# Performance work log

Hardware: AMD Instinct MI355X
Metric: run time of the kernel (lower is better)

Reference implementation:

```python
import jax, jax.numpy as jnp
import numpy as np

DIM = 1024
NUM_HEADS = 16
HEAD_DIM = DIM // NUM_HEADS
SCALE = HEAD_DIM ** -0.5


def setup_inputs() -> dict:
    key = jax.random.key(0)
    ks = jax.random.split(key, 5)
    B, N, C = 2, 2048, DIM
    x = jax.random.normal(ks[0], (B, N, C), dtype=jnp.float32)
    s = 1.0 / np.sqrt(C)
    W_qkv = jax.random.normal(ks[1], (C, 3 * C), dtype=jnp.float32) * s
    b_qkv = jax.random.normal(ks[2], (3 * C,), dtype=jnp.float32) * 0.01
    W_proj = jax.random.normal(ks[3], (C, C), dtype=jnp.float32) * s
    b_proj = jax.random.normal(ks[4], (C,), dtype=jnp.float32) * 0.01
    return {"x": x, "W_qkv": W_qkv, "b_qkv": b_qkv, "W_proj": W_proj, "b_proj": b_proj}


def reference(x, W_qkv, b_qkv, W_proj, b_proj):
    B, N, C = x.shape
    qkv = x @ W_qkv + b_qkv                      # [B, N, 3C]
    qkv = qkv.reshape(B, N, 3, NUM_HEADS, HEAD_DIM)
    qkv = jnp.transpose(qkv, (2, 0, 3, 1, 4))    # [3, B, H, N, hd]
    # Faithful to source quirk: q = k = v = qkv[2]
    v = qkv[2]
    q = v
    k = v
    attn = jnp.einsum('bhnd,bhmd->bhnm', q, k) * SCALE
    attn = jax.nn.softmax(attn, axis=-1)
    out = jnp.einsum('bhnm,bhmd->bhnd', attn, v)  # [B, H, N, hd]
    out = jnp.transpose(out, (0, 2, 1, 3)).reshape(B, N, C)
    return out @ W_proj + b_proj
```

## Files before the change

### kernel.cpp

```cpp
#include <hip/hip_runtime.h>

typedef __bf16    bf16x4 __attribute__((ext_vector_type(4)));
typedef __bf16    bf16x8 __attribute__((ext_vector_type(8)));
typedef _Float16  f16x2  __attribute__((ext_vector_type(2)));
typedef _Float16  f16x4  __attribute__((ext_vector_type(4)));
typedef _Float16  f16x8  __attribute__((ext_vector_type(8)));
typedef float     f32x4  __attribute__((ext_vector_type(4)));

#define MFMA16x16x32 __builtin_amdgcn_mfma_f32_16x16x32_bf16
#define MFMA16x16x16F __builtin_amdgcn_mfma_f32_16x16x16f16

__device__ __forceinline__ void gload_lds16(const void* g, void* l) {
  __builtin_amdgcn_global_load_lds((const __attribute__((address_space(1))) void*)g,
                                   (__attribute__((address_space(3))) void*)l, 16, 0, 0);
}

__device__ __forceinline__ f16x2 pkrtz(float a, float b) {
  return __builtin_bit_cast(f16x2, __builtin_amdgcn_cvt_pkrtz(a, b));
}

__global__ __launch_bounds__(256) void prep_transpose(const float* __restrict__ Wqkv,
                                                      const float* __restrict__ Wproj,
                                                      __bf16* __restrict__ WvT,
                                                      __bf16* __restrict__ WpT) {
  __shared__ float tile[64][65];
  const float* src; __bf16* dst; int ld, c0;
  if (blockIdx.z == 0) { src = Wqkv; dst = WvT; ld = 3072; c0 = 2048; }
  else                 { src = Wproj; dst = WpT; ld = 1024; c0 = 0; }
  const int k0 = blockIdx.x * 64, n0 = blockIdx.y * 64;
  const int t = threadIdx.x;
#pragma unroll
  for (int i = 0; i < 4; i++) {
    int idx = t + i * 256; int r = idx >> 4, g = idx & 15;
    float4 v = *(const float4*)&src[(size_t)(k0 + r) * ld + c0 + n0 + g * 4];
    tile[r][g * 4 + 0] = v.x; tile[r][g * 4 + 1] = v.y;
    tile[r][g * 4 + 2] = v.z; tile[r][g * 4 + 3] = v.w;
  }
  __syncthreads();
#pragma unroll
  for (int i = 0; i < 4; i++) {
    int idx = t + i * 256; int n = idx >> 4, g = idx & 15;
    bf16x4 o;
    o.x = (__bf16)tile[g * 4 + 0][n]; o.y = (__bf16)tile[g * 4 + 1][n];
    o.z = (__bf16)tile[g * 4 + 2][n]; o.w = (__bf16)tile[g * 4 + 3][n];
    *(bf16x4*)&dst[(size_t)(n0 + n) * 1024 + k0 + g * 4] = o;
  }
}

__global__ __launch_bounds__(256, 4) void gemm_v(const float* __restrict__ x,
                                                 const __bf16* __restrict__ WvT,
                                                 const float* __restrict__ bias,
                                                 __bf16* __restrict__ V,
                                                 _Float16* __restrict__ Vt) {
  constexpr int K = 1024;
  __shared__ char lds[2 * 12288];
  const int t = threadIdx.x, w = t >> 6, l = t & 63, lr = l & 15, quad = l >> 4;
  const int m0 = blockIdx.x * 64, n0 = blockIdx.y * 64;

  const int rmA = t >> 3;
  const int kgAs = (t & 7) ^ (rmA & 7);
  const float* pA0 = x + (size_t)(m0 + rmA) * K + kgAs * 4;
  const float* pA1 = pA0 + (size_t)32 * K;
  const int rnB = t >> 2, kgB = t & 3;
  const __bf16* pB = WvT + (size_t)(n0 + rnB) * K + kgB * 8;

  f32x4 acc[4] = {};
  {
    char* buf = (char*)lds;
    gload_lds16(pA0, buf + t * 16);
    gload_lds16(pA1, buf + (t + 256) * 16);
    gload_lds16(pB, buf + 8192 + t * 16);
  }
  const int rr = w * 16 + lr;
  const int ga0 = rr * 8 + ((2 * quad) ^ (rr & 7));
  const int ga1 = rr * 8 + ((2 * quad + 1) ^ (rr & 7));
  for (int it = 0; it < 32; ++it) {
    __syncthreads();
    if (it + 1 < 32) {
      pA0 += 32; pA1 += 32; pB += 32;
      char* buf = (char*)lds + ((it + 1) & 1) * 12288;
      gload_lds16(pA0, buf + t * 16);
      gload_lds16(pA1, buf + (t + 256) * 16);
      gload_lds16(pB, buf + 8192 + t * 16);
    }
    const char* Abuf = (char*)lds + (it & 1) * 12288;
    const char* Bbuf = Abuf + 8192;
    f32x4 a0 = *(const f32x4*)(Abuf + ga0 * 16);
    f32x4 a1 = *(const f32x4*)(Abuf + ga1 * 16);
    bf16x8 af;
    af[0] = (__bf16)a0[0]; af[1] = (__bf16)a0[1]; af[2] = (__bf16)a0[2]; af[3] = (__bf16)a0[3];
    af[4] = (__bf16)a1[0]; af[5] = (__bf16)a1[1]; af[6] = (__bf16)a1[2]; af[7] = (__bf16)a1[3];
#pragma unroll
    for (int nc = 0; nc < 4; nc++) {
      bf16x8 bv = *(const bf16x8*)(Bbuf + (nc * 16 + lr) * 64 + quad * 16);
      acc[nc] = MFMA16x16x32(af, bv, acc[nc], 0, 0, 0);
    }
  }
  const int b_ = blockIdx.x >> 5, by = blockIdx.y;
  const int ntok0 = (m0 & 2047) + w * 16 + quad * 4;
#pragma unroll
  for (int nc = 0; nc < 4; nc++) {
    int gcol = n0 + nc * 16 + lr;
    float bb = bias[gcol];
    float v0 = acc[nc][0] + bb, v1 = acc[nc][1] + bb;
    float v2 = acc[nc][2] + bb, v3 = acc[nc][3] + bb;
#pragma unroll
    for (int r = 0; r < 4; r++) {
      int grow = m0 + w * 16 + quad * 4 + r;
      float vv = (r == 0) ? v0 : (r == 1) ? v1 : (r == 2) ? v2 : v3;
      V[(size_t)grow * 1024 + gcol] = (__bf16)vv;
    }
    f16x2 lo = pkrtz(v0, v1), hi = pkrtz(v2, v3);
    f16x4 pv; pv[0] = lo[0]; pv[1] = lo[1]; pv[2] = hi[0]; pv[3] = hi[1];
    *(f16x4*)&Vt[((size_t)(b_ * 16 + by) * 64 + nc * 16 + lr) * 2048 + ntok0] = pv;
  }
}

__global__ __launch_bounds__(256, 4) void gemm_proj(const __bf16* __restrict__ A,
                                                    const __bf16* __restrict__ Bt,
                                                    const float* __restrict__ bias,
                                                    float* __restrict__ outp) {
  constexpr int K = 1024, Nn = 1024;
  __shared__ __bf16 lds[2 * 4096];
  const int t = threadIdx.x, w = t >> 6, l = t & 63, lr = l & 15, quad = l >> 4;
  const int m0 = blockIdx.x * 64, n0 = blockIdx.y * 64;
  const int rm = t >> 2, kg = t & 3;

  const __bf16* pA = A  + (size_t)(m0 + rm) * K + kg * 8;
  const __bf16* pB = Bt + (size_t)(n0 + rm) * K + kg * 8;

  f32x4 acc[4] = {};
  gload_lds16(pA, (char*)lds + t * 16);
  gload_lds16(pB, (char*)lds + 4096 + t * 16);
  for (int it = 0; it < 32; ++it) {
    __syncthreads();
    if (it + 1 < 32) {
      pA += 32; pB += 32;
      char* buf = (char*)lds + ((it + 1) & 1) * 8192;
      gload_lds16(pA, buf + t * 16);
      gload_lds16(pB, buf + 4096 + t * 16);
    }
    const __bf16* Al = lds + (it & 1) * 4096;
    const __bf16* Bl = Al + 2048;
    bf16x8 af = *(const bf16x8*)&Al[(w * 16 + lr) * 32 + quad * 8];
#pragma unroll
    for (int nc = 0; nc < 4; nc++) {
      bf16x8 bv = *(const bf16x8*)&Bl[(nc * 16 + lr) * 32 + quad * 8];
      acc[nc] = MFMA16x16x32(af, bv, acc[nc], 0, 0, 0);
    }
  }
#pragma unroll
  for (int nc = 0; nc < 4; nc++)
#pragma unroll
    for (int r = 0; r < 4; r++) {
      int grow = m0 + w * 16 + quad * 4 + r;
      int gcol = n0 + nc * 16 + lr;
      outp[(size_t)grow * Nn + gcol] = acc[nc][r] + bias[gcol];
    }
}

__global__ __launch_bounds__(512, 4) void attn_kernel(const __bf16* __restrict__ V,
                                                      const _Float16* __restrict__ Vt,
                                                      __bf16* __restrict__ O) {
  __shared__ char lds[65536];
  const int t = threadIdx.x, w = t >> 6, l = t & 63, lr = l & 15, quad = l >> 4;
  const int bh = blockIdx.x, b = bh >> 4, h = bh & 15;
  const int qb = blockIdx.y * 128 + (w & 3) * 16;
  const int part = w >> 2;

  const __bf16* Vbh = V + (size_t)b * 2048 * 1024 + h * 64;
  const _Float16* Vtbh = Vt + (size_t)bh * 64 * 2048;

  bf16x8 qf[2][2];
#pragma unroll
  for (int sub = 0; sub < 2; sub++)
#pragma unroll
    for (int ks = 0; ks < 2; ks++)
      qf[sub][ks] = *(const bf16x8*)(Vbh + (size_t)(qb + sub * 64 + lr) * 1024 + ks * 32 + quad * 8);

  const int kva = t >> 3, ua = (t & 7) ^ (kva & 7);
  const __bf16* pK0 = Vbh + (size_t)kva * 1024 + ua * 8;
  const __bf16* pK1 = pK0 + (size_t)64 * 1024;
  const int kb_ = t >> 7, d_ = (t >> 1) & 63, qh = (t & 1) ^ ((d_ >> 2) & 1);
  const _Float16* pV0 = Vtbh + (size_t)d_ * 2048 + kb_ * 16 + qh * 8;
  const _Float16* pV1 = pV0 + 64;

  const int koff0 = lr * 128 + ((quad ^ (lr & 7)) * 16);
  const int koff1 = lr * 128 + (((4 + quad) ^ (lr & 7)) * 16);
  const int xq = (quad >> 1) ^ ((lr >> 2) & 1);
  const int voff = lr * 32 + xq * 16 + (quad & 1) * 8;

  f32x4 o[2][4] = {};
  f32x4 l5[2] = {};
  f16x4 ones; ones[0] = ones[1] = ones[2] = ones[3] = (_Float16)1.0f;
  const float Cc = 0.18033688011112042f;
  const float C8 = 11.541560327111707f;

  {
    char* base = lds;
    gload_lds16(pK0, base + t * 16);
    gload_lds16(pV0, base + 8192 + t * 16);
    gload_lds16(pK1, base + 16384 + t * 16);
    gload_lds16(pV1, base + 24576 + t * 16);
  }
  for (int it = 0; it < 16; ++it) {
    __syncthreads();
    if (it + 1 < 16) {
      pK0 += 131072; pK1 += 131072; pV0 += 128; pV1 += 128;
      char* base = lds + ((it + 1) & 1) * 32768;
      gload_lds16(pK0, base + t * 16);
      gload_lds16(pV0, base + 8192 + t * 16);
      gload_lds16(pK1, base + 16384 + t * 16);
      gload_lds16(pV1, base + 24576 + t * 16);
    }
    const char* Kb = lds + (it & 1) * 32768 + part * 16384;
    const char* Vb = Kb + 8192;

    f32x4 s[2][4] = {};
#pragma unroll
    for (int ks = 0; ks < 2; ks++) {
      const int ko = ks ? koff1 : koff0;
#pragma unroll
      for (int rb = 0; rb < 4; rb++) {
        bf16x8 kf = *(const bf16x8*)(Kb + ko + rb * 2048);
        s[0][rb] = MFMA16x16x32(kf, qf[0][ks], s[0][rb], 0, 0, 0);
        s[1][rb] = MFMA16x16x32(kf, qf[1][ks], s[1][rb], 0, 0, 0);
      }
    }

    f16x4 pf[2][4];
#pragma unroll
    for (int sub = 0; sub < 2; sub++)
#pragma unroll
      for (int rb = 0; rb < 4; rb++) {
        float p0 = __builtin_amdgcn_exp2f(s[sub][rb][0] * Cc - C8);
        float p1 = __builtin_amdgcn_exp2f(s[sub][rb][1] * Cc - C8);
        float p2 = __builtin_amdgcn_exp2f(s[sub][rb][2] * Cc - C8);
        float p3 = __builtin_amdgcn_exp2f(s[sub][rb][3] * Cc - C8);
        f16x2 lo = pkrtz(p0, p1);
        f16x2 hi = pkrtz(p2, p3);
        pf[sub][rb][0] = lo[0]; pf[sub][rb][1] = lo[1];
        pf[sub][rb][2] = hi[0]; pf[sub][rb][3] = hi[1];
      }

#pragma unroll
    for (int kb = 0; kb < 4; kb++) {
#pragma unroll
      for (int db = 0; db < 4; db++) {
        f16x4 vf = *(const f16x4*)(Vb + voff + db * 512 + kb * 2048);
        o[0][db] = MFMA16x16x16F(pf[0][kb], vf, o[0][db], 0, 0, 0);
        o[1][db] = MFMA16x16x16F(pf[1][kb], vf, o[1][db], 0, 0, 0);
      }
      l5[0] = MFMA16x16x16F(pf[0][kb], ones, l5[0], 0, 0, 0);
      l5[1] = MFMA16x16x16F(pf[1][kb], ones, l5[1], 0, 0, 0);
    }
  }

  __syncthreads();
  float* xch = (float*)lds;
  if (w >= 4) {
    float* dsto = xch + (w - 4) * 2048;
#pragma unroll
    for (int sub = 0; sub < 2; sub++)
#pragma unroll
      for (int db = 0; db < 4; db++)
        *(f32x4*)&dsto[(sub * 4 + db) * 256 + l * 4] = o[sub][db];
    float* dstl = xch + 8192 + (w - 4) * 512;
    *(f32x4*)&dstl[l * 4] = l5[0];
    *(f32x4*)&dstl[256 + l * 4] = l5[1];
  }
  __syncthreads();
  if (w < 4) {
    const float* srco = xch + w * 2048;
    const float* srcl = xch + 8192 + w * 512;
#pragma unroll
    for (int sub = 0; sub < 2; sub++) {
#pragma unroll
      for (int db = 0; db < 4; db++)
        o[sub][db] += *(const f32x4*)&srco[(sub * 4 + db) * 256 + l * 4];
      l5[sub] += *(const f32x4*)&srcl[sub * 256 + l * 4];
    }
#pragma unroll
    for (int sub = 0; sub < 2; sub++)
#pragma unroll
      for (int r = 0; r < 4; r++) {
        float lv = 1.0f / l5[sub][r];
        int token = b * 2048 + qb + sub * 64 + quad * 4 + r;
#pragma unroll
        for (int db = 0; db < 4; db++)
          O[(size_t)token * 1024 + h * 64 + db * 16 + lr] = (__bf16)(o[sub][db][r] * lv);
      }
  }
}

extern "C" void kernel_launch(void* const* d_in, const int* in_sizes, int n_in,
                              void* d_out, int out_size, void* d_ws, size_t ws_size,
                              hipStream_t stream) {
  (void)in_sizes; (void)n_in; (void)out_size; (void)ws_size;
  const float* x     = (const float*)d_in[0];
  const float* Wqkv  = (const float*)d_in[1];
  const float* bqkv  = (const float*)d_in[2];
  const float* Wproj = (const float*)d_in[3];
  const float* bproj = (const float*)d_in[4];

  char* ws = (char*)d_ws;
  __bf16*    V   = (__bf16*)(ws);
  _Float16*  Vt  = (_Float16*)(ws + (size_t)8  * 1048576);
  __bf16*    Ob  = (__bf16*)(ws + (size_t)16 * 1048576);
  __bf16*    WvT = (__bf16*)(ws + (size_t)24 * 1048576);
  __bf16*    WpT = (__bf16*)(ws + (size_t)26 * 1048576);

  prep_transpose<<<dim3(16, 16, 2), 256, 0, stream>>>(Wqkv, Wproj, WvT, WpT);
  gemm_v<<<dim3(64, 16), 256, 0, stream>>>(x, WvT, bqkv + 2048, V, Vt);
  attn_kernel<<<dim3(32, 16), 512, 0, stream>>>(V, Vt, Ob);
  gemm_proj<<<dim3(64, 16), 256, 0, stream>>>(Ob, WpT, bproj, (float*)d_out);
}
```

Measured before the change: 165.1 us.

## Fuse all four stages into one persistent cooperative kernel with grid syncs

Replaces the four separate launches (weight transpose, V GEMM, attention, projection GEMM) with a single cooperative kernel of 256 blocks of 512 threads. Each phase is separated by grid.sync, and each block loops over two work tiles per phase. The GEMM tiles are retiled to 128x64. The aim is to remove launch gaps and kernel tail effects. The cost is grid-wide barriers, only 256 resident blocks, and a fallback to the old launches if the cooperative launch fails.

```diff
diff --git a/kernel.cpp b/kernel.cpp
--- a/kernel.cpp
+++ b/kernel.cpp
@@ -1,10 +1,11 @@
 #include <hip/hip_runtime.h>
+#include <hip/hip_cooperative_groups.h>
+namespace cg = cooperative_groups;
 
 typedef __bf16    bf16x4 __attribute__((ext_vector_type(4)));
 typedef __bf16    bf16x8 __attribute__((ext_vector_type(8)));
 typedef _Float16  f16x2  __attribute__((ext_vector_type(2)));
 typedef _Float16  f16x4  __attribute__((ext_vector_type(4)));
-typedef _Float16  f16x8  __attribute__((ext_vector_type(8)));
 typedef float     f32x4  __attribute__((ext_vector_type(4)));
 
 #define MFMA16x16x32 __builtin_amdgcn_mfma_f32_16x16x32_bf16
@@ -17,6 +18,284 @@
 
 __device__ __forceinline__ f16x2 pkrtz(float a, float b) {
   return __builtin_bit_cast(f16x2, __builtin_amdgcn_cvt_pkrtz(a, b));
+}
+
+__global__ __launch_bounds__(512, 2) void fused_all(
+    const float* __restrict__ x, const float* __restrict__ Wqkv,
+    const float* __restrict__ bqkv, const float* __restrict__ Wproj,
+    const float* __restrict__ bproj,
+    __bf16* __restrict__ WvT, __bf16* __restrict__ WpT,
+    __bf16* __restrict__ V, _Float16* __restrict__ Vt,
+    __bf16* __restrict__ Ob, float* __restrict__ out) {
+  __shared__ char lds[65536];
+  const int t = threadIdx.x, b = blockIdx.x;
+  const int w = t >> 6, l = t & 63, lr = l & 15, quad = l >> 4;
+  cg::grid_group grid = cg::this_grid();
+
+  for (int ii = 0; ii < 2; ii++) {
+    __syncthreads();
+    float* tile = (float*)lds;
+    const float* src; __bf16* dst; int ld, c0;
+    if (ii == 0) { src = Wqkv;  dst = WvT; ld = 3072; c0 = 2048; }
+    else         { src = Wproj; dst = WpT; ld = 1024; c0 = 0; }
+    const int k0 = (b >> 4) * 64, n0 = (b & 15) * 64;
+#pragma unroll
+    for (int i = 0; i < 2; i++) {
+      int idx = t + i * 512; int r = idx >> 4, g = idx & 15;
+      float4 v = *(const float4*)&src[(size_t)(k0 + r) * ld + c0 + n0 + g * 4];
+      tile[r * 65 + g * 4 + 0] = v.x; tile[r * 65 + g * 4 + 1] = v.y;
+      tile[r * 65 + g * 4 + 2] = v.z; tile[r * 65 + g * 4 + 3] = v.w;
+    }
+    __syncthreads();
+#pragma unroll
+    for (int i = 0; i < 2; i++) {
+      int idx = t + i * 512; int n = idx >> 4, g = idx & 15;
+      bf16x4 o;
+      o.x = (__bf16)tile[(g * 4 + 0) * 65 + n]; o.y = (__bf16)tile[(g * 4 + 1) * 65 + n];
+      o.z = (__bf16)tile[(g * 4 + 2) * 65 + n]; o.w = (__bf16)tile[(g * 4 + 3) * 65 + n];
+      *(bf16x4*)&dst[(size_t)(n0 + n) * 1024 + k0 + g * 4] = o;
+    }
+  }
+  __threadfence();
+  grid.sync();
+
+  for (int ii = 0; ii < 2; ii++) {
+    __syncthreads();
+    const int tau = b + ii * 256;
+    const int m0 = (tau >> 4) * 128, n0 = (tau & 15) * 64;
+    const int rmA = t >> 3;
+    const int kgAs = (t & 7) ^ (rmA & 7);
+    const float* pA0 = x + (size_t)(m0 + rmA) * 1024 + kgAs * 4;
+    const float* pA1 = pA0 + (size_t)64 * 1024;
+    const __bf16* pB = WvT + (size_t)(n0 + (t >> 2)) * 1024 + (t & 3) * 8;
+    f32x4 acc[4] = {};
+    {
+      char* buf = lds;
+      gload_lds16(pA0, buf + t * 16);
+      gload_lds16(pA1, buf + (t + 512) * 16);
+      if (t < 256) gload_lds16(pB, buf + 16384 + t * 16);
+    }
+    const int rr = w * 16 + lr;
+    const int ga0 = rr * 8 + ((2 * quad) ^ (rr & 7));
+    const int ga1 = rr * 8 + ((2 * quad + 1) ^ (rr & 7));
+    for (int it = 0; it < 32; ++it) {
+      __syncthreads();
+      if (it + 1 < 32) {
+        pA0 += 32; pA1 += 32; pB += 32;
+        char* buf = lds + ((it + 1) & 1) * 20480;
+        gload_lds16(pA0, buf + t * 16);
+        gload_lds16(pA1, buf + (t + 512) * 16);
+        if (t < 256) gload_lds16(pB, buf + 16384 + t * 16);
+      }
+      const char* Abuf = lds + (it & 1) * 20480;
+      const char* Bbuf = Abuf + 16384;
+      f32x4 a0 = *(const f32x4*)(Abuf + ga0 * 16);
+      f32x4 a1 = *(const f32x4*)(Abuf + ga1 * 16);
+      bf16x8 af;
+      af[0] = (__bf16)a0[0]; af[1] = (__bf16)a0[1]; af[2] = (__bf16)a0[2]; af[3] = (__bf16)a0[3];
+      af[4] = (__bf16)a1[0]; af[5] = (__bf16)a1[1]; af[6] = (__bf16)a1[2]; af[7] = (__bf16)a1[3];
+#pragma unroll
+      for (int nc = 0; nc < 4; nc++) {
+        bf16x8 bv = *(const bf16x8*)(Bbuf + (nc * 16 + lr) * 64 + quad * 16);
+        acc[nc] = MFMA16x16x32(af, bv, acc[nc], 0, 0, 0);
+      }
+    }
+    const int by = tau & 15;
+    const int b_ = m0 >> 11;
+    const int ntok0 = (m0 & 2047) + w * 16 + quad * 4;
+#pragma unroll
+    for (int nc = 0; nc < 4; nc++) {
+      int gcol = n0 + nc * 16 + lr;
+      float bb2 = bqkv[2048 + gcol];
+      float v0 = acc[nc][0] + bb2, v1 = acc[nc][1] + bb2;
+      float v2 = acc[nc][2] + bb2, v3 = acc[nc][3] + bb2;
+#pragma unroll
+      for (int r = 0; r < 4; r++) {
+        int grow = m0 + w * 16 + quad * 4 + r;
+        float vv = (r == 0) ? v0 : (r == 1) ? v1 : (r == 2) ? v2 : v3;
+        V[(size_t)grow * 1024 + gcol] = (__bf16)vv;
+      }
+      f16x2 lo = pkrtz(v0, v1), hi = pkrtz(v2, v3);
+      f16x4 pv; pv[0] = lo[0]; pv[1] = lo[1]; pv[2] = hi[0]; pv[3] = hi[1];
+      *(f16x4*)&Vt[((size_t)(b_ * 16 + by) * 64 + nc * 16 + lr) * 2048 + ntok0] = pv;
+    }
+  }
+  __threadfence();
+  grid.sync();
+
+  for (int ii = 0; ii < 2; ii++) {
+    __syncthreads();
+    const int u = b + ii * 256;
+    const int bh = u & 31, bb = bh >> 4, h = bh & 15;
+    const int qb = (u >> 5) * 128 + (w & 3) * 16;
+    const int part = w >> 2;
+
+    const __bf16* Vbh = V + (size_t)bb * 2048 * 1024 + h * 64;
+    const _Float16* Vtbh = Vt + (size_t)bh * 64 * 2048;
+
+    bf16x8 qf[2][2];
+#pragma unroll
+    for (int sub = 0; sub < 2; sub++)
+#pragma unroll
+      for (int ks = 0; ks < 2; ks++)
+        qf[sub][ks] = *(const bf16x8*)(Vbh + (size_t)(qb + sub * 64 + lr) * 1024 + ks * 32 + quad * 8);
+
+    const int kva = t >> 3, ua = (t & 7) ^ (kva & 7);
+    const __bf16* pK0 = Vbh + (size_t)kva * 1024 + ua * 8;
+    const __bf16* pK1 = pK0 + (size_t)64 * 1024;
+    const int kb_ = t >> 7, d_ = (t >> 1) & 63, qh = (t & 1) ^ ((d_ >> 2) & 1);
+    const _Float16* pV0 = Vtbh + (size_t)d_ * 2048 + kb_ * 16 + qh * 8;
+    const _Float16* pV1 = pV0 + 64;
+
+    const int koff0 = lr * 128 + ((quad ^ (lr & 7)) * 16);
+    const int koff1 = lr * 128 + (((4 + quad) ^ (lr & 7)) * 16);
+    const int xq = (quad >> 1) ^ ((lr >> 2) & 1);
+    const int voff = lr * 32 + xq * 16 + (quad & 1) * 8;
+
+    f32x4 o[2][4] = {};
+    f32x4 l5[2] = {};
+    f16x4 ones; ones[0] = ones[1] = ones[2] = ones[3] = (_Float16)1.0f;
+    const float Cc = 0.18033688011112042f;
+    const float C8 = 11.541560327111707f;
+
+    {
+      char* base = lds;
+      gload_lds16(pK0, base + t * 16);
+      gload_lds16(pV0, base + 8192 + t * 16);
+      gload_lds16(pK1, base + 16384 + t * 16);
+      gload_lds16(pV1, base + 24576 + t * 16);
+    }
+    for (int it = 0; it < 16; ++it) {
+      __syncthreads();
+      if (it + 1 < 16) {
+        pK0 += 131072; pK1 += 131072; pV0 += 128; pV1 += 128;
+        char* base = lds + ((it + 1) & 1) * 32768;
+        gload_lds16(pK0, base + t * 16);
+        gload_lds16(pV0, base + 8192 + t * 16);
+        gload_lds16(pK1, base + 16384 + t * 16);
+        gload_lds16(pV1, base + 24576 + t * 16);
+      }
+      const char* Kb = lds + (it & 1) * 32768 + part * 16384;
+      const char* Vb = Kb + 8192;
+
+      f32x4 s[2][4] = {};
+#pragma unroll
+      for (int ks = 0; ks < 2; ks++) {
+        const int ko = ks ? koff1 : koff0;
+#pragma unroll
+        for (int rb = 0; rb < 4; rb++) {
+          bf16x8 kf = *(const bf16x8*)(Kb + ko + rb * 2048);
+          s[0][rb] = MFMA16x16x32(kf, qf[0][ks], s[0][rb], 0, 0, 0);
+          s[1][rb] = MFMA16x16x32(kf, qf[1][ks], s[1][rb], 0, 0, 0);
+        }
+      }
+
+      f16x4 pf[2][4];
+#pragma unroll
+      for (int sub = 0; sub < 2; sub++)
+#pragma unroll
+        for (int rb = 0; rb < 4; rb++) {
+          float p0 = __builtin_amdgcn_exp2f(s[sub][rb][0] * Cc - C8);
+          float p1 = __builtin_amdgcn_exp2f(s[sub][rb][1] * Cc - C8);
+          float p2 = __builtin_amdgcn_exp2f(s[sub][rb][2] * Cc - C8);
+          float p3 = __builtin_amdgcn_exp2f(s[sub][rb][3] * Cc - C8);
+          f16x2 lo = pkrtz(p0, p1);
+          f16x2 hi = pkrtz(p2, p3);
+          pf[sub][rb][0] = lo[0]; pf[sub][rb][1] = lo[1];
+          pf[sub][rb][2] = hi[0]; pf[sub][rb][3] = hi[1];
+        }
+
+#pragma unroll
+      for (int kb = 0; kb < 4; kb++) {
+#pragma unroll
+        for (int db = 0; db < 4; db++) {
+          f16x4 vf = *(const f16x4*)(Vb + voff + db * 512 + kb * 2048);
+          o[0][db] = MFMA16x16x16F(pf[0][kb], vf, o[0][db], 0, 0, 0);
+          o[1][db] = MFMA16x16x16F(pf[1][kb], vf, o[1][db], 0, 0, 0);
+        }
+        l5[0] = MFMA16x16x16F(pf[0][kb], ones, l5[0], 0, 0, 0);
+        l5[1] = MFMA16x16x16F(pf[1][kb], ones, l5[1], 0, 0, 0);
+      }
+    }
+
+    __syncthreads();
+    float* xch = (float*)lds;
+    if (w >= 4) {
+      float* dsto = xch + (w - 4) * 2048;
+#pragma unroll
+      for (int sub = 0; sub < 2; sub++)
+#pragma unroll
+        for (int db = 0; db < 4; db++)
+          *(f32x4*)&dsto[(sub * 4 + db) * 256 + l * 4] = o[sub][db];
+      float* dstl = xch + 8192 + (w - 4) * 512;
+      *(f32x4*)&dstl[l * 4] = l5[0];
+      *(f32x4*)&dstl[256 + l * 4] = l5[1];
+    }
+    __syncthreads();
+    if (w < 4) {
+      const float* srco = xch + w * 2048;
+      const float* srcl = xch + 8192 + w * 512;
+#pragma unroll
+      for (int sub = 0; sub < 2; sub++) {
+#pragma unroll
+        for (int db = 0; db < 4; db++)
+          o[sub][db] += *(const f32x4*)&srco[(sub * 4 + db) * 256 + l * 4];
+        l5[sub] += *(const f32x4*)&srcl[sub * 256 + l * 4];
+      }
+#pragma unroll
+      for (int sub = 0; sub < 2; sub++)
+#pragma unroll
+        for (int r = 0; r < 4; r++) {
+          float lv = 1.0f / l5[sub][r];
+          int token = bb * 2048 + qb + sub * 64 + quad * 4 + r;
+#pragma unroll
+          for (int db = 0; db < 4; db++)
+            Ob[(size_t)token * 1024 + h * 64 + db * 16 + lr] = (__bf16)(o[sub][db][r] * lv);
+        }
+    }
+  }
+  __threadfence();
+  grid.sync();
+
+  for (int ii = 0; ii < 2; ii++) {
+    __syncthreads();
+    const int tau = b + ii * 256;
+    const int m0 = (tau >> 4) * 128, n0 = (tau & 15) * 64;
+    const __bf16* pA = Ob + (size_t)(m0 + (t >> 2)) * 1024 + (t & 3) * 8;
+    const __bf16* pB = WpT + (size_t)(n0 + (t >> 2)) * 1024 + (t & 3) * 8;
+    f32x4 acc[4] = {};
+    {
+      char* buf = lds;
+      gload_lds16(pA, buf + t * 16);
+      if (t < 256) gload_lds16(pB, buf + 8192 + t * 16);
+    }
+    const int rr = w * 16 + lr;
+    for (int it = 0; it < 32; ++it) {
+      __syncthreads();
+      if (it + 1 < 32) {
+        pA += 32; pB += 32;
+        char* buf = lds + ((it + 1) & 1) * 12288;
+        gload_lds16(pA, buf + t * 16);
+        if (t < 256) gload_lds16(pB, buf + 8192 + t * 16);
+      }
+      const char* Abuf = lds + (it & 1) * 12288;
+      const char* Bbuf = Abuf + 8192;
+      bf16x8 af = *(const bf16x8*)(Abuf + rr * 64 + quad * 16);
+#pragma unroll
+      for (int nc = 0; nc < 4; nc++) {
+        bf16x8 bv = *(const bf16x8*)(Bbuf + (nc * 16 + lr) * 64 + quad * 16);
+        acc[nc] = MFMA16x16x32(af, bv, acc[nc], 0, 0, 0);
+      }
+    }
+#pragma unroll
+    for (int nc = 0; nc < 4; nc++)
+#pragma unroll
+      for (int r = 0; r < 4; r++) {
+        int grow = m0 + w * 16 + quad * 4 + r;
+        int gcol = n0 + nc * 16 + lr;
+        out[(size_t)grow * 1024 + gcol] = acc[nc][r] + bproj[gcol];
+      }
+  }
 }
 
 __global__ __launch_bounds__(256) void prep_transpose(const float* __restrict__ Wqkv,
@@ -56,7 +335,6 @@
   __shared__ char lds[2 * 12288];
   const int t = threadIdx.x, w = t >> 6, l = t & 63, lr = l & 15, quad = l >> 4;
   const int m0 = blockIdx.x * 64, n0 = blockIdx.y * 64;
-
   const int rmA = t >> 3;
   const int kgAs = (t & 7) ^ (rmA & 7);
   const float* pA0 = x + (size_t)(m0 + rmA) * K + kgAs * 4;
@@ -125,10 +403,8 @@
   const int t = threadIdx.x, w = t >> 6, l = t & 63, lr = l & 15, quad = l >> 4;
   const int m0 = blockIdx.x * 64, n0 = blockIdx.y * 64;
   const int rm = t >> 2, kg = t & 3;
-
   const __bf16* pA = A  + (size_t)(m0 + rm) * K + kg * 8;
   const __bf16* pB = Bt + (size_t)(n0 + rm) * K + kg * 8;
-
   f32x4 acc[4] = {};
   gload_lds16(pA, (char*)lds + t * 16);
   gload_lds16(pB, (char*)lds + 4096 + t * 16);
@@ -167,35 +443,29 @@
   const int bh = blockIdx.x, b = bh >> 4, h = bh & 15;
   const int qb = blockIdx.y * 128 + (w & 3) * 16;
   const int part = w >> 2;
-
   const __bf16* Vbh = V + (size_t)b * 2048 * 1024 + h * 64;
   const _Float16* Vtbh = Vt + (size_t)bh * 64 * 2048;
-
   bf16x8 qf[2][2];
 #pragma unroll
   for (int sub = 0; sub < 2; sub++)
 #pragma unroll
     for (int ks = 0; ks < 2; ks++)
       qf[sub][ks] = *(const bf16x8*)(Vbh + (size_t)(qb + sub * 64 + lr) * 1024 + ks * 32 + quad * 8);
-
   const int kva = t >> 3, ua = (t & 7) ^ (kva & 7);
   const __bf16* pK0 = Vbh + (size_t)kva * 1024 + ua * 8;
   const __bf16* pK1 = pK0 + (size_t)64 * 1024;
   const int kb_ = t >> 7, d_ = (t >> 1) & 63, qh = (t & 1) ^ ((d_ >> 2) & 1);
   const _Float16* pV0 = Vtbh + (size_t)d_ * 2048 + kb_ * 16 + qh * 8;
   const _Float16* pV1 = pV0 + 64;
-
   const int koff0 = lr * 128 + ((quad ^ (lr & 7)) * 16);
   const int koff1 = lr * 128 + (((4 + quad) ^ (lr & 7)) * 16);
   const int xq = (quad >> 1) ^ ((lr >> 2) & 1);
   const int voff = lr * 32 + xq * 16 + (quad & 1) * 8;
-
   f32x4 o[2][4] = {};
   f32x4 l5[2] = {};
   f16x4 ones; ones[0] = ones[1] = ones[2] = ones[3] = (_Float16)1.0f;
   const float Cc = 0.18033688011112042f;
   const float C8 = 11.541560327111707f;
-
   {
     char* base = lds;
     gload_lds16(pK0, base + t * 16);
@@ -215,7 +485,6 @@
     }
     const char* Kb = lds + (it & 1) * 32768 + part * 16384;
     const char* Vb = Kb + 8192;
-
     f32x4 s[2][4] = {};
 #pragma unroll
     for (int ks = 0; ks < 2; ks++) {
@@ -227,7 +496,6 @@
         s[1][rb] = MFMA16x16x32(kf, qf[1][ks], s[1][rb], 0, 0, 0);
       }
     }
-
     f16x4 pf[2][4];
 #pragma unroll
     for (int sub = 0; sub < 2; sub++)
@@ -242,7 +510,6 @@
         pf[sub][rb][0] = lo[0]; pf[sub][rb][1] = lo[1];
         pf[sub][rb][2] = hi[0]; pf[sub][rb][3] = hi[1];
       }
-
 #pragma unroll
     for (int kb = 0; kb < 4; kb++) {
 #pragma unroll
@@ -255,7 +522,6 @@
       l5[1] = MFMA16x16x16F(pf[1][kb], ones, l5[1], 0, 0, 0);
     }
   }
-
   __syncthreads();
   float* xch = (float*)lds;
   if (w >= 4) {
@@ -309,9 +575,16 @@
   __bf16*    Ob  = (__bf16*)(ws + (size_t)16 * 1048576);
   __bf16*    WvT = (__bf16*)(ws + (size_t)24 * 1048576);
   __bf16*    WpT = (__bf16*)(ws + (size_t)26 * 1048576);
-
-  prep_transpose<<<dim3(16, 16, 2), 256, 0, stream>>>(Wqkv, Wproj, WvT, WpT);
-  gemm_v<<<dim3(64, 16), 256, 0, stream>>>(x, WvT, bqkv + 2048, V, Vt);
-  attn_kernel<<<dim3(32, 16), 512, 0, stream>>>(V, Vt, Ob);
-  gemm_proj<<<dim3(64, 16), 256, 0, stream>>>(Ob, WpT, bproj, (float*)d_out);
-}
+  float*     out = (float*)d_out;
+
+  void* args[] = {&x, &Wqkv, &bqkv, &Wproj, &bproj, &WvT, &WpT, &V, &Vt, &Ob, &out};
+  hipError_t err = hipLaunchCooperativeKernel((void*)fused_all, dim3(256), dim3(512),
+                                              args, 0, stream);
+  if (err != hipSuccess) {
+    (void)hipGetLastError();
+    prep_transpose<<<dim3(16, 16, 2), 256, 0, stream>>>(Wqkv, Wproj, WvT, WpT);
+    gemm_v<<<dim3(64, 16), 256, 0, stream>>>(x, WvT, bqkv + 2048, V, Vt);
+    attn_kernel<<<dim3(32, 16), 512, 0, stream>>>(V, Vt, Ob);
+    gemm_proj<<<dim3(64, 16), 256, 0, stream>>>(Ob, WpT, bproj, out);
+  }
+}
```

Result: slower. 426.7 us (+158.4%).
